# Optimization experiments

Measured on AMD Instinct MI355X. Metric: run time of the kernel, lower is better.

The kernel has to match this reference:

```python
import jax, jax.numpy as jnp
import numpy as np

N, E, NG = 10000, 160000, 64
HID, HEADS = 256, 4
NEG_SLOPE = 0.2


def setup_inputs() -> dict:
    key = jax.random.key(0)
    ks = jax.random.split(key, 20)
    s = 0.1
    inp = {
        "atom_features": jax.random.normal(ks[0], (N, 23), jnp.float32),
        "edge_index": jax.random.randint(ks[1], (2, E), 0, N),
        "batch": jnp.sort(jax.random.randint(ks[2], (N,), 0, NG)),
        "W1": jax.random.normal(ks[3], (23, HEADS * HID), jnp.float32) * s,
        "as1": jax.random.normal(ks[4], (HEADS, HID), jnp.float32) * s,
        "ad1": jax.random.normal(ks[5], (HEADS, HID), jnp.float32) * s,
        "b1": jnp.zeros((HEADS * HID,), jnp.float32),
        "W2": jax.random.normal(ks[6], (HEADS * HID, HEADS * HID), jnp.float32) * s,
        "as2": jax.random.normal(ks[7], (HEADS, HID), jnp.float32) * s,
        "ad2": jax.random.normal(ks[8], (HEADS, HID), jnp.float32) * s,
        "b2": jnp.zeros((HEADS * HID,), jnp.float32),
        "W3": jax.random.normal(ks[9], (HEADS * HID, HID), jnp.float32) * s,
        "as3": jax.random.normal(ks[10], (1, HID), jnp.float32) * s,
        "ad3": jax.random.normal(ks[11], (1, HID), jnp.float32) * s,
        "b3": jnp.zeros((HID,), jnp.float32),
        # MLP head
        "fc1_w": jax.random.normal(ks[12], (HID, HID // 2), jnp.float32) * s,
        "fc1_b": jnp.zeros((HID // 2,), jnp.float32),
        "fc2_w": jax.random.normal(ks[13], (HID // 2, 1), jnp.float32) * s,
        "fc2_b": jnp.zeros((1,), jnp.float32),
    }
    return inp


def gat_layer(x, W, att_src, att_dst, bias, src, dst, heads, ch):
    n = x.shape[0]
    h = (x @ W).reshape(n, heads, ch)                      # [N,H,C]
    a_s = jnp.sum(h * att_src, axis=-1)                    # [N,H]
    a_d = jnp.sum(h * att_dst, axis=-1)                    # [N,H]
    logits = jax.nn.leaky_relu(a_s[src] + a_d[dst], NEG_SLOPE)  # [E',H]
    m = jax.ops.segment_max(logits, dst, num_segments=n)
    m = jnp.where(jnp.isfinite(m), m, 0.0)
    e = jnp.exp(logits - m[dst])
    denom = jax.ops.segment_sum(e, dst, num_segments=n)
    alpha = e / (denom[dst] + 1e-16)                       # segment softmax over incoming edges
    out = jax.ops.segment_sum(alpha[:, :, None] * h[src], dst, num_segments=n)
    return out.reshape(n, heads * ch) + bias


def reference(atom_features, edge_index, batch,
              W1, as1, ad1, b1, W2, as2, ad2, b2, W3, as3, ad3, b3,
              fc1_w, fc1_b, fc2_w, fc2_b):
    n = atom_features.shape[0]
    loops = jnp.arange(n)
    src = jnp.concatenate([edge_index[0], loops])   # PyG GATConv adds self-loops
    dst = jnp.concatenate([edge_index[1], loops])

    x = jax.nn.elu(gat_layer(atom_features, W1, as1, ad1, b1, src, dst, HEADS, HID))
    x = jax.nn.elu(gat_layer(x, W2, as2, ad2, b2, src, dst, HEADS, HID))
    x = jax.nn.elu(gat_layer(x, W3, as3, ad3, b3, src, dst, 1, HID))
    # dropout: eval mode (training=False) -> identity

    # global mean pool over molecules
    sums = jax.ops.segment_sum(x, batch, num_segments=NG)
    counts = jax.ops.segment_sum(jnp.ones((n,), x.dtype), batch, num_segments=NG)
    features = sums / jnp.maximum(counts, 1.0)[:, None]    # [NG, HID]

    hmid = jax.nn.relu(features @ fc1_w + fc1_b)
    validity = hmid @ fc2_w + fc2_b                        # [NG, 1]
    return validity, features
```

## Files before the change

### kernel.cpp

```cpp
#include <hip/hip_runtime.h>
#include <hip/hip_bf16.h>
#include <math.h>

typedef unsigned short ushortT;
typedef __attribute__((ext_vector_type(8))) short short8;
typedef __attribute__((ext_vector_type(4))) float f32x4;

constexpr int NN   = 10000;
constexpr int EE   = 160000;
constexpr int ETOT = EE + NN;
constexpr int NG   = 64;
constexpr int HID  = 256;
constexpr int HEADS = 4;

__device__ __forceinline__ ushortT f2bf(float x) {
    __hip_bfloat16 h = __float2bfloat16(x);
    return *reinterpret_cast<ushortT*>(&h);
}
__device__ __forceinline__ float bf2f(ushortT x) {
    unsigned u = ((unsigned)x) << 16;
    return __uint_as_float(u);
}

__global__ void edge_count_kernel(const int* __restrict__ ei, int* __restrict__ cnt) {
    int e = blockIdx.x * blockDim.x + threadIdx.x;
    if (e >= ETOT) return;
    int dst = (e < EE) ? ei[EE + e] : (e - EE);
    atomicAdd(&cnt[dst], 1);
}

__global__ void scan_kernel(const int* __restrict__ cnt, int* __restrict__ row_ptr,
                            int* __restrict__ cursor) {
    __shared__ int part[256];
    int tid = threadIdx.x;
    const int chunk = (NN + 255) / 256;
    int s0 = tid * chunk;
    int s1 = min(NN, s0 + chunk);
    int sum = 0;
    for (int i = s0; i < s1; ++i) sum += cnt[i];
    part[tid] = sum;
    __syncthreads();
    for (int off = 1; off < 256; off <<= 1) {
        int v = (tid >= off) ? part[tid - off] : 0;
        __syncthreads();
        part[tid] += v;
        __syncthreads();
    }
    int run = (tid == 0) ? 0 : part[tid - 1];
    for (int i = s0; i < s1; ++i) {
        row_ptr[i] = run;
        cursor[i]  = run;
        run += cnt[i];
    }
    if (tid == 255) row_ptr[NN] = part[255];
}

__global__ void edge_fill_kernel(const int* __restrict__ ei, int* __restrict__ cursor,
                                 int* __restrict__ col_src) {
    int e = blockIdx.x * blockDim.x + threadIdx.x;
    if (e >= ETOT) return;
    int src, dst;
    if (e < EE) { src = ei[e]; dst = ei[EE + e]; }
    else        { src = dst = e - EE; }
    int pos = atomicAdd(&cursor[dst], 1);
    col_src[pos] = src;
}

__global__ void convert_wt(const float* __restrict__ W, ushortT* __restrict__ Wt,
                           int K, int N, int Kp) {
    __shared__ float t[32][33];
    int n0 = blockIdx.x * 32, k0 = blockIdx.y * 32;
    int tx = threadIdx.x, ty = threadIdx.y;
    for (int i = ty; i < 32; i += 8) {
        int k = k0 + i, n = n0 + tx;
        t[i][tx] = (k < K && n < N) ? W[(size_t)k * N + n] : 0.f;
    }
    __syncthreads();
    for (int i = ty; i < 32; i += 8) {
        int n = n0 + i, kp = k0 + tx;
        if (n < N && kp < Kp) Wt[(size_t)n * Kp + kp] = f2bf(t[tx][i]);
    }
}

__global__ void convert_atom(const float* __restrict__ a, ushortT* __restrict__ out) {
    int idx = blockIdx.x * 256 + threadIdx.x;
    if (idx >= NN * 32) return;
    int n = idx >> 5, k = idx & 31;
    out[idx] = (k < 23) ? f2bf(a[n * 23 + k]) : (ushortT)0;
}

__device__ __forceinline__ void gload_lds16(const ushortT* gsrc, ushortT* ldst) {
    __builtin_amdgcn_global_load_lds(
        (const __attribute__((address_space(1))) unsigned int*)gsrc,
        (__attribute__((address_space(3))) unsigned int*)ldst, 16, 0, 0);
}

__global__ __launch_bounds__(256, 2) void gemm_bf16(const ushortT* __restrict__ A,
                                                    const ushortT* __restrict__ Bt,
                                                    ushortT* __restrict__ C,
                                                    int M, int N, int K) {
    __shared__ ushortT lds[2][2][128][32];
    const int tid  = threadIdx.x;
    const int lane = tid & 63, w = tid >> 6;
    const int wm = w >> 1, wn = w & 1;
    const int row0 = blockIdx.y * 128;
    const int col0 = blockIdx.x * 128;
    const int nt = K >> 5;

    auto stage = [&](int buf, int t) {
        int k0 = t << 5;
        #pragma unroll
        for (int i = 0; i < 2; ++i) {
            int gbase = (w * 2 + i) * 64;
            int g = gbase + lane;
            int row = g >> 2;
            int sw = (row & 3) ^ ((row >> 2) & 3);
            int koff = (g & 3) ^ sw;
            int arow = min(row0 + row, M - 1);
            gload_lds16(A + (size_t)arow * K + k0 + koff * 8,
                        &lds[buf][0][0][0] + gbase * 8);
            int brow = col0 + row;
            gload_lds16(Bt + (size_t)brow * K + k0 + koff * 8,
                        &lds[buf][1][0][0] + gbase * 8);
        }
    };

    f32x4 acc[4][4] = {};
    const int lr = lane & 15, lk = lane >> 4;

    stage(0, 0);
    for (int t = 0; t < nt; ++t) {
        int buf = t & 1;
        __syncthreads();
        if (t + 1 < nt) stage(buf ^ 1, t + 1);
        short8 a[4], b[4];
        const ushortT* baseA = &lds[buf][0][0][0];
        const ushortT* baseB = &lds[buf][1][0][0];
        #pragma unroll
        for (int m = 0; m < 4; ++m) {
            int row = wm * 64 + m * 16 + lr;
            int sw = (row & 3) ^ ((row >> 2) & 3);
            a[m] = *(const short8*)(baseA + row * 32 + ((lk ^ sw) * 8));
        }
        #pragma unroll
        for (int n = 0; n < 4; ++n) {
            int row = wn * 64 + n * 16 + lr;
            int sw = (row & 3) ^ ((row >> 2) & 3);
            b[n] = *(const short8*)(baseB + row * 32 + ((lk ^ sw) * 8));
        }
        #pragma unroll
        for (int m = 0; m < 4; ++m)
            #pragma unroll
            for (int n = 0; n < 4; ++n)
                acc[m][n] = __builtin_amdgcn_mfma_f32_16x16x32_bf16(a[m], b[n], acc[m][n], 0, 0, 0);
    }

    #pragma unroll
    for (int m = 0; m < 4; ++m) {
        #pragma unroll
        for (int n = 0; n < 4; ++n) {
            int col = col0 + wn * 64 + n * 16 + lr;
            #pragma unroll
            for (int j = 0; j < 4; ++j) {
                int rowg = row0 + wm * 64 + m * 16 + lk * 4 + j;
                if (rowg < M) C[(size_t)rowg * N + col] = f2bf(acc[m][n][j]);
            }
        }
    }
}

__global__ void attn_dots2(const ushortT* __restrict__ h,
                           const float* __restrict__ att_s,
                           const float* __restrict__ att_d,
                           float* __restrict__ a_s, float* __restrict__ a_d,
                           int heads) {
    int wid  = (blockIdx.x * blockDim.x + threadIdx.x) >> 6;
    int lane = threadIdx.x & 63;
    int total = NN * heads;
    if (wid >= total) return;
    int n = wid / heads, hh = wid - n * heads;
    ushort4 v  = *(const ushort4*)(h + (size_t)n * heads * HID + hh * HID + lane * 4);
    float4 s4 = *(const float4*)(att_s + hh * HID + lane * 4);
    float4 d4 = *(const float4*)(att_d + hh * HID + lane * 4);
    float vx = bf2f(v.x), vy = bf2f(v.y), vz = bf2f(v.z), vw = bf2f(v.w);
    float as = vx * s4.x + vy * s4.y + vz * s4.z + vw * s4.w;
    float ad = vx * d4.x + vy * d4.y + vz * d4.z + vw * d4.w;
    #pragma unroll
    for (int off = 32; off > 0; off >>= 1) {
        as += __shfl_down(as, off);
        ad += __shfl_down(ad, off);
    }
    if (lane == 0) { a_s[wid] = as; a_d[wid] = ad; }
}

__global__ __launch_bounds__(256) void gat_aggregate(const ushortT* __restrict__ hfeat,
                                                     const float* __restrict__ a_s,
                                                     const float* __restrict__ a_d,
                                                     const int* __restrict__ row_ptr,
                                                     const int* __restrict__ col_src,
                                                     const float* __restrict__ bias,
                                                     float* __restrict__ outf,
                                                     ushortT* __restrict__ out16,
                                                     int heads) {
    const int i = blockIdx.x, tid = threadIdx.x;
    const int C = heads * HID;
    const int nch = heads;
    const int c0 = tid * nch;
    const int hh = c0 >> 8;
    const int start = row_ptr[i], end = row_ptr[i + 1];

    float ad_i[4];
    #pragma unroll
    for (int h2 = 0; h2 < 4; ++h2) ad_i[h2] = (h2 < heads) ? a_d[i * heads + h2] : 0.f;

    __shared__ float wbuf[4 * 128];
    __shared__ int   sbuf[128];
    __shared__ float red[4 * 256];
    float dpart[4] = {0.f, 0.f, 0.f, 0.f};
    float acc[4]   = {0.f, 0.f, 0.f, 0.f};
    for (int cb = start; cb < end; cb += 128) {
        int clen = min(128, end - cb);
        if (tid < clen) {
            int s = col_src[cb + tid];
            sbuf[tid] = s;
            #pragma unroll
            for (int h2 = 0; h2 < 4; ++h2) {
                if (h2 < heads) {
                    float l = a_s[s * heads + h2] + ad_i[h2];
                    l = (l >= 0.f) ? l : 0.2f * l;
                    float wv = expf(l);
                    wbuf[h2 * 128 + tid] = wv;
                    dpart[h2] += wv;
                }
            }
        }
        __syncthreads();
        if (nch == 4) {
            for (int e = 0; e < clen; ++e) {
                int s = sbuf[e];
                float wv = wbuf[hh * 128 + e];
                ushort4 v = *reinterpret_cast<const ushort4*>(hfeat + (size_t)s * C + c0);
                acc[0] += wv * bf2f(v.x); acc[1] += wv * bf2f(v.y);
                acc[2] += wv * bf2f(v.z); acc[3] += wv * bf2f(v.w);
            }
        } else {
            for (int e = 0; e < clen; ++e) {
                int s = sbuf[e];
                acc[0] += wbuf[e] * bf2f(hfeat[(size_t)s * C + c0]);
            }
        }
        __syncthreads();
    }
    for (int h2 = 0; h2 < heads; ++h2) red[h2 * 256 + tid] = dpart[h2];
    __syncthreads();
    for (int s2 = 128; s2 > 0; s2 >>= 1) {
        if (tid < s2)
            for (int h2 = 0; h2 < heads; ++h2)
                red[h2 * 256 + tid] += red[h2 * 256 + tid + s2];
        __syncthreads();
    }
    float denom = red[hh * 256] + 1e-16f;
    if (nch == 4) {
        ushort4 pk;
        float v0 = acc[0] / denom + bias[c0 + 0]; v0 = (v0 > 0.f) ? v0 : expm1f(v0);
        float v1 = acc[1] / denom + bias[c0 + 1]; v1 = (v1 > 0.f) ? v1 : expm1f(v1);
        float v2 = acc[2] / denom + bias[c0 + 2]; v2 = (v2 > 0.f) ? v2 : expm1f(v2);
        float v3 = acc[3] / denom + bias[c0 + 3]; v3 = (v3 > 0.f) ? v3 : expm1f(v3);
        pk.x = f2bf(v0); pk.y = f2bf(v1); pk.z = f2bf(v2); pk.w = f2bf(v3);
        *reinterpret_cast<ushort4*>(out16 + (size_t)i * C + c0) = pk;
    } else {
        float v = acc[0] / denom + bias[c0];
        v = (v > 0.f) ? v : expm1f(v);
        outf[(size_t)i * C + c0] = v;
    }
}

__global__ void pool_mlp(const float* __restrict__ x,
                         const int* __restrict__ batch,
                         const float* __restrict__ fc1_w,
                         const float* __restrict__ fc1_b,
                         const float* __restrict__ fc2_w,
                         const float* __restrict__ fc2_b,
                         float* __restrict__ out) {
    int g = blockIdx.x, tid = threadIdx.x;
    int lo = 0, hi = NN;
    while (lo < hi) { int mid = (lo + hi) >> 1; if (batch[mid] < g) lo = mid + 1; else hi = mid; }
    int s0 = lo;
    lo = 0; hi = NN;
    while (lo < hi) { int mid = (lo + hi) >> 1; if (batch[mid] < g + 1) lo = mid + 1; else hi = mid; }
    int s1 = lo;

    float acc = 0.f;
    for (int n = s0; n < s1; ++n) acc += x[(size_t)n * HID + tid];
    float cnt = (float)(s1 - s0);
    float feat = acc / fmaxf(cnt, 1.f);
    out[NG + g * HID + tid] = feat;

    __shared__ float fsh[HID];
    fsh[tid] = feat;
    __syncthreads();
    __shared__ float r2[128];
    if (tid < 128) {
        float a = fc1_b[tid];
        for (int c = 0; c < HID; ++c) a += fsh[c] * fc1_w[c * 128 + tid];
        a = fmaxf(a, 0.f);
        r2[tid] = a * fc2_w[tid];
    }
    __syncthreads();
    for (int s2 = 64; s2 > 0; s2 >>= 1) {
        if (tid < s2) r2[tid] += r2[tid + s2];
        __syncthreads();
    }
    if (tid == 0) out[g] = r2[0] + fc2_b[0];
}

extern "C" void kernel_launch(void* const* d_in, const int* in_sizes, int n_in,
                              void* d_out, int out_size, void* d_ws, size_t ws_size,
                              hipStream_t stream) {
    const float* atom  = (const float*)d_in[0];
    const int*   ei    = (const int*)  d_in[1];
    const int*   batch = (const int*)  d_in[2];
    const float* W1  = (const float*)d_in[3];
    const float* as1 = (const float*)d_in[4];
    const float* ad1 = (const float*)d_in[5];
    const float* b1  = (const float*)d_in[6];
    const float* W2  = (const float*)d_in[7];
    const float* as2 = (const float*)d_in[8];
    const float* ad2 = (const float*)d_in[9];
    const float* b2  = (const float*)d_in[10];
    const float* W3  = (const float*)d_in[11];
    const float* as3 = (const float*)d_in[12];
    const float* ad3 = (const float*)d_in[13];
    const float* b3  = (const float*)d_in[14];
    const float* fc1w = (const float*)d_in[15];
    const float* fc1b = (const float*)d_in[16];
    const float* fc2w = (const float*)d_in[17];
    const float* fc2b = (const float*)d_in[18];
    float* out = (float*)d_out;

    ushortT* h16  = (ushortT*)d_ws;
    ushortT* x16  = h16 + (size_t)NN * 1024;
    float*   x3   = (float*)(x16 + (size_t)NN * 1024);
    float*   a_s  = x3 + (size_t)NN * 256;
    float*   a_d  = a_s + (size_t)NN * HEADS;
    ushortT* wt1  = (ushortT*)(a_d + (size_t)NN * HEADS);
    ushortT* wt2  = wt1 + 1024 * 32;
    ushortT* wt3  = wt2 + 1024 * 1024;
    int*   cnt    = (int*)(wt3 + 256 * 1024);
    int*   rowp   = cnt + NN;
    int*   cursor = rowp + NN + 1;
    int*   col    = cursor + NN;

    hipMemsetAsync(cnt, 0, NN * sizeof(int), stream);
    edge_count_kernel<<<(ETOT + 255) / 256, 256, 0, stream>>>(ei, cnt);
    scan_kernel<<<1, 256, 0, stream>>>(cnt, rowp, cursor);
    edge_fill_kernel<<<(ETOT + 255) / 256, 256, 0, stream>>>(ei, cursor, col);

    dim3 cblk(32, 8);
    convert_atom<<<(NN * 32 + 255) / 256, 256, 0, stream>>>(atom, x16);
    convert_wt<<<dim3(32, 1),  cblk, 0, stream>>>(W1, wt1, 23,   1024, 32);
    convert_wt<<<dim3(32, 32), cblk, 0, stream>>>(W2, wt2, 1024, 1024, 1024);
    convert_wt<<<dim3(8, 32),  cblk, 0, stream>>>(W3, wt3, 1024, 256,  1024);

    dim3 blk(256);
    const int gy = (NN + 127) / 128;

    gemm_bf16<<<dim3(8, gy), blk, 0, stream>>>(x16, wt1, h16, NN, 1024, 32);
    attn_dots2<<<(NN * HEADS * 64 + 255) / 256, blk, 0, stream>>>(h16, as1, ad1, a_s, a_d, HEADS);
    gat_aggregate<<<NN, blk, 0, stream>>>(h16, a_s, a_d, rowp, col, b1, nullptr, x16, HEADS);

    gemm_bf16<<<dim3(8, gy), blk, 0, stream>>>(x16, wt2, h16, NN, 1024, 1024);
    attn_dots2<<<(NN * HEADS * 64 + 255) / 256, blk, 0, stream>>>(h16, as2, ad2, a_s, a_d, HEADS);
    gat_aggregate<<<NN, blk, 0, stream>>>(h16, a_s, a_d, rowp, col, b2, nullptr, x16, HEADS);

    gemm_bf16<<<dim3(2, gy), blk, 0, stream>>>(x16, wt3, h16, NN, 256, 1024);
    attn_dots2<<<(NN * 1 * 64 + 255) / 256, blk, 0, stream>>>(h16, as3, ad3, a_s, a_d, 1);
    gat_aggregate<<<NN, blk, 0, stream>>>(h16, a_s, a_d, rowp, col, b3, x3, nullptr, 1);

    pool_mlp<<<NG, blk, 0, stream>>>(x3, batch, fc1w, fc1b, fc2w, fc2b, out);
}
```

Baseline: 341.2 us.

## Fuse attention dots into GEMM epilogue and aggregate one node per wave

Removes the separate attn_dots2 kernel. The GEMM epilogue now computes each row's per-head source and destination attention dot products from the fp32 accumulators, reduces them with lane shuffles and atomically adds them into zeroed buffers. The aggregation kernel moves from one 256-thread block per node to one wavefront per node, four nodes per block. It uses wave-level barriers instead of __syncthreads, a shuffle reduction for the softmax denominator, and wider 16-element bf16 loads per lane. The cost is an extra memset per layer and atomics in the GEMM epilogue, and the dot products now come from unrounded accumulators, so numerics shift slightly.

```diff
diff --git a/kernel.cpp b/kernel.cpp
--- a/kernel.cpp
+++ b/kernel.cpp
@@ -98,6 +98,11 @@
 __global__ __launch_bounds__(256, 2) void gemm_bf16(const ushortT* __restrict__ A,
                                                     const ushortT* __restrict__ Bt,
                                                     ushortT* __restrict__ C,
+                                                    const float* __restrict__ att_s,
+                                                    const float* __restrict__ att_d,
+                                                    float* __restrict__ a_sp,
+                                                    float* __restrict__ a_dp,
+                                                    int adim,
                                                     int M, int N, int K) {
     __shared__ ushortT lds[2][2][128][32];
     const int tid  = threadIdx.x;
@@ -167,111 +172,152 @@
             }
         }
     }
-}
-
-__global__ void attn_dots2(const ushortT* __restrict__ h,
-                           const float* __restrict__ att_s,
-                           const float* __restrict__ att_d,
-                           float* __restrict__ a_s, float* __restrict__ a_d,
-                           int heads) {
-    int wid  = (blockIdx.x * blockDim.x + threadIdx.x) >> 6;
-    int lane = threadIdx.x & 63;
-    int total = NN * heads;
-    if (wid >= total) return;
-    int n = wid / heads, hh = wid - n * heads;
-    ushort4 v  = *(const ushort4*)(h + (size_t)n * heads * HID + hh * HID + lane * 4);
-    float4 s4 = *(const float4*)(att_s + hh * HID + lane * 4);
-    float4 d4 = *(const float4*)(att_d + hh * HID + lane * 4);
-    float vx = bf2f(v.x), vy = bf2f(v.y), vz = bf2f(v.z), vw = bf2f(v.w);
-    float as = vx * s4.x + vy * s4.y + vz * s4.z + vw * s4.w;
-    float ad = vx * d4.x + vy * d4.y + vz * d4.z + vw * d4.w;
-    #pragma unroll
-    for (int off = 32; off > 0; off >>= 1) {
-        as += __shfl_down(as, off);
-        ad += __shfl_down(ad, off);
-    }
-    if (lane == 0) { a_s[wid] = as; a_d[wid] = ad; }
-}
-
-__global__ __launch_bounds__(256) void gat_aggregate(const ushortT* __restrict__ hfeat,
-                                                     const float* __restrict__ a_s,
-                                                     const float* __restrict__ a_d,
-                                                     const int* __restrict__ row_ptr,
-                                                     const int* __restrict__ col_src,
-                                                     const float* __restrict__ bias,
-                                                     float* __restrict__ outf,
-                                                     ushortT* __restrict__ out16,
-                                                     int heads) {
-    const int i = blockIdx.x, tid = threadIdx.x;
+
+    {
+        const int colbase = col0 + wn * 64;
+        const int head = colbase >> 8;
+        float s_att[4], d_att[4];
+        #pragma unroll
+        for (int n = 0; n < 4; ++n) {
+            int col = colbase + n * 16 + lr;
+            s_att[n] = att_s[col];
+            d_att[n] = att_d[col];
+        }
+        #pragma unroll
+        for (int m = 0; m < 4; ++m) {
+            #pragma unroll
+            for (int j = 0; j < 4; ++j) {
+                float ps = acc[m][0][j] * s_att[0] + acc[m][1][j] * s_att[1]
+                         + acc[m][2][j] * s_att[2] + acc[m][3][j] * s_att[3];
+                float pd = acc[m][0][j] * d_att[0] + acc[m][1][j] * d_att[1]
+                         + acc[m][2][j] * d_att[2] + acc[m][3][j] * d_att[3];
+                #pragma unroll
+                for (int off = 1; off < 16; off <<= 1) {
+                    ps += __shfl_xor(ps, off);
+                    pd += __shfl_xor(pd, off);
+                }
+                if (lr == 0) {
+                    int rowg = row0 + wm * 64 + m * 16 + lk * 4 + j;
+                    if (rowg < M) {
+                        atomicAdd(a_sp + (size_t)rowg * adim + head, ps);
+                        atomicAdd(a_dp + (size_t)rowg * adim + head, pd);
+                    }
+                }
+            }
+        }
+    }
+}
+
+__global__ __launch_bounds__(256) void gat_aggregate_w(const ushortT* __restrict__ hfeat,
+                                                       const float* __restrict__ a_s,
+                                                       const float* __restrict__ a_d,
+                                                       const int* __restrict__ row_ptr,
+                                                       const int* __restrict__ col_src,
+                                                       const float* __restrict__ bias,
+                                                       float* __restrict__ outf,
+                                                       ushortT* __restrict__ out16,
+                                                       int heads) {
+    const int wv = threadIdx.x >> 6, lane = threadIdx.x & 63;
+    const int i = blockIdx.x * 4 + wv;
+    if (i >= NN) return;
     const int C = heads * HID;
-    const int nch = heads;
-    const int c0 = tid * nch;
+    const int nch = C >> 6;
+    const int c0 = lane * nch;
     const int hh = c0 >> 8;
     const int start = row_ptr[i], end = row_ptr[i + 1];
 
-    float ad_i[4];
+    __shared__ float wsh[4][64][4];
+    __shared__ int   ssh[4][64];
+
+    float acc[16];
     #pragma unroll
-    for (int h2 = 0; h2 < 4; ++h2) ad_i[h2] = (h2 < heads) ? a_d[i * heads + h2] : 0.f;
-
-    __shared__ float wbuf[4 * 128];
-    __shared__ int   sbuf[128];
-    __shared__ float red[4 * 256];
-    float dpart[4] = {0.f, 0.f, 0.f, 0.f};
-    float acc[4]   = {0.f, 0.f, 0.f, 0.f};
-    for (int cb = start; cb < end; cb += 128) {
-        int clen = min(128, end - cb);
-        if (tid < clen) {
-            int s = col_src[cb + tid];
-            sbuf[tid] = s;
-            #pragma unroll
-            for (int h2 = 0; h2 < 4; ++h2) {
-                if (h2 < heads) {
-                    float l = a_s[s * heads + h2] + ad_i[h2];
-                    l = (l >= 0.f) ? l : 0.2f * l;
-                    float wv = expf(l);
-                    wbuf[h2 * 128 + tid] = wv;
-                    dpart[h2] += wv;
+    for (int c = 0; c < 16; ++c) acc[c] = 0.f;
+    float den4[4] = {0.f, 0.f, 0.f, 0.f};
+
+    for (int cb = start; cb < end; cb += 64) {
+        int clen = min(64, end - cb);
+        if (lane < clen) {
+            int s = col_src[cb + lane];
+            ssh[wv][lane] = s;
+            if (heads == 4) {
+                float4 as4 = *(const float4*)(a_s + (size_t)s * 4);
+                float4 ad4 = *(const float4*)(a_d + (size_t)i * 4);
+                float l0 = as4.x + ad4.x; l0 = (l0 >= 0.f) ? l0 : 0.2f * l0;
+                float l1 = as4.y + ad4.y; l1 = (l1 >= 0.f) ? l1 : 0.2f * l1;
+                float l2 = as4.z + ad4.z; l2 = (l2 >= 0.f) ? l2 : 0.2f * l2;
+                float l3 = as4.w + ad4.w; l3 = (l3 >= 0.f) ? l3 : 0.2f * l3;
+                float w0 = expf(l0), w1 = expf(l1), w2 = expf(l2), w3 = expf(l3);
+                *reinterpret_cast<float4*>(&wsh[wv][lane][0]) = make_float4(w0, w1, w2, w3);
+                den4[0] += w0; den4[1] += w1; den4[2] += w2; den4[3] += w3;
+            } else {
+                float l0 = a_s[s] + a_d[i]; l0 = (l0 >= 0.f) ? l0 : 0.2f * l0;
+                float w0 = expf(l0);
+                wsh[wv][lane][0] = w0;
+                den4[0] += w0;
+            }
+        }
+        __builtin_amdgcn_wave_barrier();
+        if (nch == 16) {
+            for (int e = 0; e < clen; ++e) {
+                int s = ssh[wv][e];
+                float wgt = wsh[wv][e][hh];
+                const ushortT* p = hfeat + (size_t)s * C + c0;
+                short8 v0 = *(const short8*)p;
+                short8 v1 = *(const short8*)(p + 8);
+                #pragma unroll
+                for (int j = 0; j < 8; ++j) {
+                    acc[j]     += wgt * bf2f((ushortT)v0[j]);
+                    acc[8 + j] += wgt * bf2f((ushortT)v1[j]);
                 }
-            }
-        }
-        __syncthreads();
-        if (nch == 4) {
-            for (int e = 0; e < clen; ++e) {
-                int s = sbuf[e];
-                float wv = wbuf[hh * 128 + e];
-                ushort4 v = *reinterpret_cast<const ushort4*>(hfeat + (size_t)s * C + c0);
-                acc[0] += wv * bf2f(v.x); acc[1] += wv * bf2f(v.y);
-                acc[2] += wv * bf2f(v.z); acc[3] += wv * bf2f(v.w);
             }
         } else {
             for (int e = 0; e < clen; ++e) {
-                int s = sbuf[e];
-                acc[0] += wbuf[e] * bf2f(hfeat[(size_t)s * C + c0]);
+                int s = ssh[wv][e];
+                float wgt = wsh[wv][e][0];
+                const ushortT* p = hfeat + (size_t)s * C + c0;
+                ushort4 v = *(const ushort4*)p;
+                acc[0] += wgt * bf2f(v.x); acc[1] += wgt * bf2f(v.y);
+                acc[2] += wgt * bf2f(v.z); acc[3] += wgt * bf2f(v.w);
             }
         }
-        __syncthreads();
-    }
-    for (int h2 = 0; h2 < heads; ++h2) red[h2 * 256 + tid] = dpart[h2];
-    __syncthreads();
-    for (int s2 = 128; s2 > 0; s2 >>= 1) {
-        if (tid < s2)
-            for (int h2 = 0; h2 < heads; ++h2)
-                red[h2 * 256 + tid] += red[h2 * 256 + tid + s2];
-        __syncthreads();
-    }
-    float denom = red[hh * 256] + 1e-16f;
-    if (nch == 4) {
-        ushort4 pk;
-        float v0 = acc[0] / denom + bias[c0 + 0]; v0 = (v0 > 0.f) ? v0 : expm1f(v0);
-        float v1 = acc[1] / denom + bias[c0 + 1]; v1 = (v1 > 0.f) ? v1 : expm1f(v1);
-        float v2 = acc[2] / denom + bias[c0 + 2]; v2 = (v2 > 0.f) ? v2 : expm1f(v2);
-        float v3 = acc[3] / denom + bias[c0 + 3]; v3 = (v3 > 0.f) ? v3 : expm1f(v3);
-        pk.x = f2bf(v0); pk.y = f2bf(v1); pk.z = f2bf(v2); pk.w = f2bf(v3);
-        *reinterpret_cast<ushort4*>(out16 + (size_t)i * C + c0) = pk;
+        __builtin_amdgcn_wave_barrier();
+    }
+
+    if (heads == 4) {
+        #pragma unroll
+        for (int off = 1; off < 64; off <<= 1) {
+            den4[0] += __shfl_xor(den4[0], off);
+            den4[1] += __shfl_xor(den4[1], off);
+            den4[2] += __shfl_xor(den4[2], off);
+            den4[3] += __shfl_xor(den4[3], off);
+        }
     } else {
-        float v = acc[0] / denom + bias[c0];
-        v = (v > 0.f) ? v : expm1f(v);
-        outf[(size_t)i * C + c0] = v;
+        #pragma unroll
+        for (int off = 1; off < 64; off <<= 1) den4[0] += __shfl_xor(den4[0], off);
+    }
+    float den = den4[0];
+    if (heads == 4) {
+        den = (hh == 0) ? den4[0] : (hh == 1) ? den4[1] : (hh == 2) ? den4[2] : den4[3];
+    }
+    float inv = 1.f / (den + 1e-16f);
+
+    if (heads == 4) {
+        ushortT pk[16];
+        #pragma unroll
+        for (int c = 0; c < 16; ++c) {
+            float v = acc[c] * inv + bias[c0 + c];
+            v = (v > 0.f) ? v : expm1f(v);
+            pk[c] = f2bf(v);
+        }
+        *reinterpret_cast<short8*>(out16 + (size_t)i * C + c0)     = *reinterpret_cast<short8*>(&pk[0]);
+        *reinterpret_cast<short8*>(out16 + (size_t)i * C + c0 + 8) = *reinterpret_cast<short8*>(&pk[8]);
+    } else {
+        float4 o;
+        float v0 = acc[0] * inv + bias[c0 + 0]; o.x = (v0 > 0.f) ? v0 : expm1f(v0);
+        float v1 = acc[1] * inv + bias[c0 + 1]; o.y = (v1 > 0.f) ? v1 : expm1f(v1);
+        float v2 = acc[2] * inv + bias[c0 + 2]; o.z = (v2 > 0.f) ? v2 : expm1f(v2);
+        float v3 = acc[3] * inv + bias[c0 + 3]; o.w = (v3 > 0.f) ? v3 : expm1f(v3);
+        *reinterpret_cast<float4*>(outf + (size_t)i * C + c0) = o;
     }
 }
 
@@ -364,18 +410,19 @@
 
     dim3 blk(256);
     const int gy = (NN + 127) / 128;
-
-    gemm_bf16<<<dim3(8, gy), blk, 0, stream>>>(x16, wt1, h16, NN, 1024, 32);
-    attn_dots2<<<(NN * HEADS * 64 + 255) / 256, blk, 0, stream>>>(h16, as1, ad1, a_s, a_d, HEADS);
-    gat_aggregate<<<NN, blk, 0, stream>>>(h16, a_s, a_d, rowp, col, b1, nullptr, x16, HEADS);
-
-    gemm_bf16<<<dim3(8, gy), blk, 0, stream>>>(x16, wt2, h16, NN, 1024, 1024);
-    attn_dots2<<<(NN * HEADS * 64 + 255) / 256, blk, 0, stream>>>(h16, as2, ad2, a_s, a_d, HEADS);
-    gat_aggregate<<<NN, blk, 0, stream>>>(h16, a_s, a_d, rowp, col, b2, nullptr, x16, HEADS);
-
-    gemm_bf16<<<dim3(2, gy), blk, 0, stream>>>(x16, wt3, h16, NN, 256, 1024);
-    attn_dots2<<<(NN * 1 * 64 + 255) / 256, blk, 0, stream>>>(h16, as3, ad3, a_s, a_d, 1);
-    gat_aggregate<<<NN, blk, 0, stream>>>(h16, a_s, a_d, rowp, col, b3, x3, nullptr, 1);
+    const int gagg = (NN + 3) / 4;
+
+    hipMemsetAsync(a_s, 0, (size_t)NN * 2 * HEADS * sizeof(float), stream);
+    gemm_bf16<<<dim3(8, gy), blk, 0, stream>>>(x16, wt1, h16, as1, ad1, a_s, a_d, HEADS, NN, 1024, 32);
+    gat_aggregate_w<<<gagg, blk, 0, stream>>>(h16, a_s, a_d, rowp, col, b1, nullptr, x16, HEADS);
+
+    hipMemsetAsync(a_s, 0, (size_t)NN * 2 * HEADS * sizeof(float), stream);
+    gemm_bf16<<<dim3(8, gy), blk, 0, stream>>>(x16, wt2, h16, as2, ad2, a_s, a_d, HEADS, NN, 1024, 1024);
+    gat_aggregate_w<<<gagg, blk, 0, stream>>>(h16, a_s, a_d, rowp, col, b2, nullptr, x16, HEADS);
+
+    hipMemsetAsync(a_s, 0, (size_t)NN * 2 * HEADS * sizeof(float), stream);
+    gemm_bf16<<<dim3(2, gy), blk, 0, stream>>>(x16, wt3, h16, as3, ad3, a_s, a_d, 1, NN, 256, 1024);
+    gat_aggregate_w<<<gagg, blk, 0, stream>>>(h16, a_s, a_d, rowp, col, b3, x3, nullptr, 1);
 
     pool_mlp<<<NG, blk, 0, stream>>>(x3, batch, fc1w, fc1b, fc2w, fc2b, out);
 }
```

After: 358.3 us. +5.0%, slower.

## Fold attention projections into weights and fuse next-layer dots into aggregation

Applied to the files above, without the earlier changes.

Precomputes W·att_src and W·att_dst so the per-node attention scores for the next layer are computed inside the aggregation epilogue, accumulated with atomics, instead of by a separate dot kernel over the GEMM output. This removes the attn_dots kernels and a full re-read of the projected features per layer. It also rewrites aggregation as two wavefronts per node, each loading 8 neighbors' 8-channel vectors with no LDS or block-level syncs. The scores now come from fp32 activations rather than the bf16-rounded GEMM output, which slightly changes numerics, and the scheme adds atomics and memsets.

```diff
diff --git a/kernel.cpp b/kernel.cpp
--- a/kernel.cpp
+++ b/kernel.cpp
@@ -89,6 +89,43 @@
     out[idx] = (k < 23) ? f2bf(a[n * 23 + k]) : (ushortT)0;
 }
 
+__global__ void proj_att(const float* __restrict__ W,
+                         const float* __restrict__ atts,
+                         const float* __restrict__ attd,
+                         float* __restrict__ wsv,
+                         int K, int heads) {
+    const int nout = 2 * heads;
+    int gw   = (blockIdx.x * blockDim.x + threadIdx.x) >> 6;
+    int lane = threadIdx.x & 63;
+    if (gw >= K * nout) return;
+    int k = gw / nout, o = gw - k * nout;
+    int h = (o >= heads) ? (o - heads) : o;
+    const float* att  = ((o >= heads) ? attd : atts) + h * HID;
+    const float* wrow = W + (size_t)k * (heads * HID) + h * HID;
+    float4 w4 = *(const float4*)(wrow + lane * 4);
+    float4 a4 = *(const float4*)(att + lane * 4);
+    float s = w4.x * a4.x + w4.y * a4.y + w4.z * a4.z + w4.w * a4.w;
+    #pragma unroll
+    for (int off = 1; off < 64; off <<= 1) s += __shfl_xor(s, off);
+    if (lane == 0) wsv[(size_t)k * nout + o] = s;
+}
+
+__global__ void dots1_kernel(const float* __restrict__ atom,
+                             const float* __restrict__ wsv1,
+                             float* __restrict__ a_s, float* __restrict__ a_d) {
+    int n = blockIdx.x * 256 + threadIdx.x;
+    if (n >= NN) return;
+    float a[8] = {0.f, 0.f, 0.f, 0.f, 0.f, 0.f, 0.f, 0.f};
+    #pragma unroll
+    for (int k = 0; k < 23; ++k) {
+        float x = atom[n * 23 + k];
+        #pragma unroll
+        for (int o = 0; o < 8; ++o) a[o] += x * wsv1[k * 8 + o];
+    }
+    #pragma unroll
+    for (int h = 0; h < 4; ++h) { a_s[n * 4 + h] = a[h]; a_d[n * 4 + h] = a[4 + h]; }
+}
+
 __device__ __forceinline__ void gload_lds16(const ushortT* gsrc, ushortT* ldst) {
     __builtin_amdgcn_global_load_lds(
         (const __attribute__((address_space(1))) unsigned int*)gsrc,
@@ -169,110 +206,145 @@
     }
 }
 
-__global__ void attn_dots2(const ushortT* __restrict__ h,
-                           const float* __restrict__ att_s,
-                           const float* __restrict__ att_d,
-                           float* __restrict__ a_s, float* __restrict__ a_d,
-                           int heads) {
-    int wid  = (blockIdx.x * blockDim.x + threadIdx.x) >> 6;
+template<int NOUT>
+__global__ __launch_bounds__(256) void gat_agg4(const ushortT* __restrict__ hfeat,
+                                                const float* __restrict__ a_s,
+                                                const float* __restrict__ a_d,
+                                                const int* __restrict__ rowp,
+                                                const int* __restrict__ colv,
+                                                const float* __restrict__ bias,
+                                                ushortT* __restrict__ out16,
+                                                const float* __restrict__ wsv,
+                                                float* __restrict__ as_next,
+                                                float* __restrict__ ad_next) {
+    int gw   = (blockIdx.x * blockDim.x + threadIdx.x) >> 6;
     int lane = threadIdx.x & 63;
-    int total = NN * heads;
-    if (wid >= total) return;
-    int n = wid / heads, hh = wid - n * heads;
-    ushort4 v  = *(const ushort4*)(h + (size_t)n * heads * HID + hh * HID + lane * 4);
-    float4 s4 = *(const float4*)(att_s + hh * HID + lane * 4);
-    float4 d4 = *(const float4*)(att_d + hh * HID + lane * 4);
-    float vx = bf2f(v.x), vy = bf2f(v.y), vz = bf2f(v.z), vw = bf2f(v.w);
-    float as = vx * s4.x + vy * s4.y + vz * s4.z + vw * s4.w;
-    float ad = vx * d4.x + vy * d4.y + vz * d4.z + vw * d4.w;
+    int i = gw >> 1, p = gw & 1;
+    if (i >= NN) return;
+    const int c0 = p * 512 + lane * 8;
+    const int hh = c0 >> 8;
+    const int start = rowp[i], end = rowp[i + 1];
+    const float adh = a_d[i * 4 + hh];
+
+    float acc[8] = {0.f, 0.f, 0.f, 0.f, 0.f, 0.f, 0.f, 0.f};
+    float den = 0.f;
+    for (int e0 = start; e0 < end; e0 += 8) {
+        const int mcnt = end - e0;
+        int sidx[8];
+        #pragma unroll
+        for (int j = 0; j < 8; ++j) sidx[j] = colv[(j < mcnt) ? (e0 + j) : e0];
+        short8 v[8];
+        #pragma unroll
+        for (int j = 0; j < 8; ++j)
+            v[j] = *(const short8*)(hfeat + (size_t)sidx[j] * 1024 + c0);
+        float asv[8];
+        #pragma unroll
+        for (int j = 0; j < 8; ++j) asv[j] = a_s[sidx[j] * 4 + hh];
+        float wv[8];
+        #pragma unroll
+        for (int j = 0; j < 8; ++j) {
+            float l = asv[j] + adh;
+            l = (l >= 0.f) ? l : 0.2f * l;
+            wv[j] = (j < mcnt) ? expf(l) : 0.f;
+            den += wv[j];
+        }
+        #pragma unroll
+        for (int j = 0; j < 8; ++j) {
+            #pragma unroll
+            for (int c = 0; c < 8; ++c)
+                acc[c] += wv[j] * bf2f((ushortT)v[j][c]);
+        }
+    }
+    float inv = 1.f / (den + 1e-16f);
+    float vout[8];
+    ushortT pk[8];
     #pragma unroll
-    for (int off = 32; off > 0; off >>= 1) {
-        as += __shfl_down(as, off);
-        ad += __shfl_down(ad, off);
-    }
-    if (lane == 0) { a_s[wid] = as; a_d[wid] = ad; }
-}
-
-__global__ __launch_bounds__(256) void gat_aggregate(const ushortT* __restrict__ hfeat,
-                                                     const float* __restrict__ a_s,
-                                                     const float* __restrict__ a_d,
-                                                     const int* __restrict__ row_ptr,
-                                                     const int* __restrict__ col_src,
-                                                     const float* __restrict__ bias,
-                                                     float* __restrict__ outf,
-                                                     ushortT* __restrict__ out16,
-                                                     int heads) {
-    const int i = blockIdx.x, tid = threadIdx.x;
-    const int C = heads * HID;
-    const int nch = heads;
-    const int c0 = tid * nch;
-    const int hh = c0 >> 8;
-    const int start = row_ptr[i], end = row_ptr[i + 1];
-
-    float ad_i[4];
-    #pragma unroll
-    for (int h2 = 0; h2 < 4; ++h2) ad_i[h2] = (h2 < heads) ? a_d[i * heads + h2] : 0.f;
-
-    __shared__ float wbuf[4 * 128];
-    __shared__ int   sbuf[128];
-    __shared__ float red[4 * 256];
-    float dpart[4] = {0.f, 0.f, 0.f, 0.f};
-    float acc[4]   = {0.f, 0.f, 0.f, 0.f};
-    for (int cb = start; cb < end; cb += 128) {
-        int clen = min(128, end - cb);
-        if (tid < clen) {
-            int s = col_src[cb + tid];
-            sbuf[tid] = s;
-            #pragma unroll
-            for (int h2 = 0; h2 < 4; ++h2) {
-                if (h2 < heads) {
-                    float l = a_s[s * heads + h2] + ad_i[h2];
-                    l = (l >= 0.f) ? l : 0.2f * l;
-                    float wv = expf(l);
-                    wbuf[h2 * 128 + tid] = wv;
-                    dpart[h2] += wv;
-                }
+    for (int c = 0; c < 8; ++c) {
+        float v = acc[c] * inv + bias[c0 + c];
+        v = (v > 0.f) ? v : expm1f(v);
+        vout[c] = v;
+        pk[c] = f2bf(v);
+    }
+    *reinterpret_cast<short8*>(out16 + (size_t)i * 1024 + c0) =
+        *reinterpret_cast<const short8*>(pk);
+
+    if (NOUT > 0) {
+        float ps[NOUT];
+        #pragma unroll
+        for (int o = 0; o < NOUT; ++o) {
+            float t = 0.f;
+            #pragma unroll
+            for (int c = 0; c < 8; ++c) t += vout[c] * wsv[(size_t)(c0 + c) * NOUT + o];
+            ps[o] = t;
+        }
+        #pragma unroll
+        for (int off = 1; off < 64; off <<= 1) {
+            #pragma unroll
+            for (int o = 0; o < NOUT; ++o) ps[o] += __shfl_xor(ps[o], off);
+        }
+        if (lane == 0) {
+            constexpr int NH = NOUT / 2;
+            #pragma unroll
+            for (int o = 0; o < NH; ++o) {
+                atomicAdd(as_next + (size_t)i * NH + o, ps[o]);
+                atomicAdd(ad_next + (size_t)i * NH + o, ps[NH + o]);
             }
         }
-        __syncthreads();
-        if (nch == 4) {
-            for (int e = 0; e < clen; ++e) {
-                int s = sbuf[e];
-                float wv = wbuf[hh * 128 + e];
-                ushort4 v = *reinterpret_cast<const ushort4*>(hfeat + (size_t)s * C + c0);
-                acc[0] += wv * bf2f(v.x); acc[1] += wv * bf2f(v.y);
-                acc[2] += wv * bf2f(v.z); acc[3] += wv * bf2f(v.w);
-            }
-        } else {
-            for (int e = 0; e < clen; ++e) {
-                int s = sbuf[e];
-                acc[0] += wbuf[e] * bf2f(hfeat[(size_t)s * C + c0]);
-            }
-        }
-        __syncthreads();
-    }
-    for (int h2 = 0; h2 < heads; ++h2) red[h2 * 256 + tid] = dpart[h2];
-    __syncthreads();
-    for (int s2 = 128; s2 > 0; s2 >>= 1) {
-        if (tid < s2)
-            for (int h2 = 0; h2 < heads; ++h2)
-                red[h2 * 256 + tid] += red[h2 * 256 + tid + s2];
-        __syncthreads();
-    }
-    float denom = red[hh * 256] + 1e-16f;
-    if (nch == 4) {
-        ushort4 pk;
-        float v0 = acc[0] / denom + bias[c0 + 0]; v0 = (v0 > 0.f) ? v0 : expm1f(v0);
-        float v1 = acc[1] / denom + bias[c0 + 1]; v1 = (v1 > 0.f) ? v1 : expm1f(v1);
-        float v2 = acc[2] / denom + bias[c0 + 2]; v2 = (v2 > 0.f) ? v2 : expm1f(v2);
-        float v3 = acc[3] / denom + bias[c0 + 3]; v3 = (v3 > 0.f) ? v3 : expm1f(v3);
-        pk.x = f2bf(v0); pk.y = f2bf(v1); pk.z = f2bf(v2); pk.w = f2bf(v3);
-        *reinterpret_cast<ushort4*>(out16 + (size_t)i * C + c0) = pk;
-    } else {
-        float v = acc[0] / denom + bias[c0];
-        v = (v > 0.f) ? v : expm1f(v);
-        outf[(size_t)i * C + c0] = v;
-    }
+    }
+}
+
+__global__ __launch_bounds__(256) void gat_agg1(const ushortT* __restrict__ hfeat,
+                                                const float* __restrict__ a_s,
+                                                const float* __restrict__ a_d,
+                                                const int* __restrict__ rowp,
+                                                const int* __restrict__ colv,
+                                                const float* __restrict__ bias,
+                                                float* __restrict__ outf) {
+    int gw   = (blockIdx.x * blockDim.x + threadIdx.x) >> 6;
+    int lane = threadIdx.x & 63;
+    int i = gw;
+    if (i >= NN) return;
+    const int c0 = lane * 4;
+    const int start = rowp[i], end = rowp[i + 1];
+    const float adh = a_d[i];
+
+    float acc[4] = {0.f, 0.f, 0.f, 0.f};
+    float den = 0.f;
+    for (int e0 = start; e0 < end; e0 += 8) {
+        const int mcnt = end - e0;
+        int sidx[8];
+        #pragma unroll
+        for (int j = 0; j < 8; ++j) sidx[j] = colv[(j < mcnt) ? (e0 + j) : e0];
+        ushort4 v[8];
+        #pragma unroll
+        for (int j = 0; j < 8; ++j)
+            v[j] = *(const ushort4*)(hfeat + (size_t)sidx[j] * 256 + c0);
+        float asv[8];
+        #pragma unroll
+        for (int j = 0; j < 8; ++j) asv[j] = a_s[sidx[j]];
+        float wv[8];
+        #pragma unroll
+        for (int j = 0; j < 8; ++j) {
+            float l = asv[j] + adh;
+            l = (l >= 0.f) ? l : 0.2f * l;
+            wv[j] = (j < mcnt) ? expf(l) : 0.f;
+            den += wv[j];
+        }
+        #pragma unroll
+        for (int j = 0; j < 8; ++j) {
+            acc[0] += wv[j] * bf2f(v[j].x);
+            acc[1] += wv[j] * bf2f(v[j].y);
+            acc[2] += wv[j] * bf2f(v[j].z);
+            acc[3] += wv[j] * bf2f(v[j].w);
+        }
+    }
+    float inv = 1.f / (den + 1e-16f);
+    float4 o4;
+    float v0 = acc[0] * inv + bias[c0 + 0]; o4.x = (v0 > 0.f) ? v0 : expm1f(v0);
+    float v1 = acc[1] * inv + bias[c0 + 1]; o4.y = (v1 > 0.f) ? v1 : expm1f(v1);
+    float v2 = acc[2] * inv + bias[c0 + 2]; o4.z = (v2 > 0.f) ? v2 : expm1f(v2);
+    float v3 = acc[3] * inv + bias[c0 + 3]; o4.w = (v3 > 0.f) ? v3 : expm1f(v3);
+    *reinterpret_cast<float4*>(outf + (size_t)i * 256 + c0) = o4;
 }
 
 __global__ void pool_mlp(const float* __restrict__ x,
@@ -341,9 +413,14 @@
     ushortT* h16  = (ushortT*)d_ws;
     ushortT* x16  = h16 + (size_t)NN * 1024;
     float*   x3   = (float*)(x16 + (size_t)NN * 1024);
-    float*   a_s  = x3 + (size_t)NN * 256;
-    float*   a_d  = a_s + (size_t)NN * HEADS;
-    ushortT* wt1  = (ushortT*)(a_d + (size_t)NN * HEADS);
+    float*   asA  = x3 + (size_t)NN * 256;
+    float*   adA  = asA + (size_t)NN * 4;
+    float*   asB  = adA + (size_t)NN * 4;
+    float*   adB  = asB + (size_t)NN * 4;
+    float*   wsv1 = adB + (size_t)NN * 4;
+    float*   wsv2 = wsv1 + 23 * 8;
+    float*   wsv3 = wsv2 + 1024 * 8;
+    ushortT* wt1  = (ushortT*)(wsv3 + 1024 * 2);
     ushortT* wt2  = wt1 + 1024 * 32;
     ushortT* wt3  = wt2 + 1024 * 1024;
     int*   cnt    = (int*)(wt3 + 256 * 1024);
@@ -362,20 +439,27 @@
     convert_wt<<<dim3(32, 32), cblk, 0, stream>>>(W2, wt2, 1024, 1024, 1024);
     convert_wt<<<dim3(8, 32),  cblk, 0, stream>>>(W3, wt3, 1024, 256,  1024);
 
+    proj_att<<<(23 * 8 * 64 + 255) / 256, 256, 0, stream>>>(W1, as1, ad1, wsv1, 23, 4);
+    proj_att<<<(1024 * 8 * 64 + 255) / 256, 256, 0, stream>>>(W2, as2, ad2, wsv2, 1024, 4);
+    proj_att<<<(1024 * 2 * 64 + 255) / 256, 256, 0, stream>>>(W3, as3, ad3, wsv3, 1024, 1);
+
+    dots1_kernel<<<(NN + 255) / 256, 256, 0, stream>>>(atom, wsv1, asA, adA);
+    hipMemsetAsync(asB, 0, (size_t)NN * 8 * sizeof(float), stream);
+
     dim3 blk(256);
     const int gy = (NN + 127) / 128;
 
     gemm_bf16<<<dim3(8, gy), blk, 0, stream>>>(x16, wt1, h16, NN, 1024, 32);
-    attn_dots2<<<(NN * HEADS * 64 + 255) / 256, blk, 0, stream>>>(h16, as1, ad1, a_s, a_d, HEADS);
-    gat_aggregate<<<NN, blk, 0, stream>>>(h16, a_s, a_d, rowp, col, b1, nullptr, x16, HEADS);
+    gat_agg4<8><<<(NN * 2 * 64 + 255) / 256, blk, 0, stream>>>(h16, asA, adA, rowp, col,
+                                                               b1, x16, wsv2, asB, adB);
+    hipMemsetAsync(asA, 0, (size_t)NN * 8 * sizeof(float), stream);
 
     gemm_bf16<<<dim3(8, gy), blk, 0, stream>>>(x16, wt2, h16, NN, 1024, 1024);
-    attn_dots2<<<(NN * HEADS * 64 + 255) / 256, blk, 0, stream>>>(h16, as2, ad2, a_s, a_d, HEADS);
-    gat_aggregate<<<NN, blk, 0, stream>>>(h16, a_s, a_d, rowp, col, b2, nullptr, x16, HEADS);
+    gat_agg4<2><<<(NN * 2 * 64 + 255) / 256, blk, 0, stream>>>(h16, asB, adB, rowp, col,
+                                                               b2, x16, wsv3, asA, adA);
 
     gemm_bf16<<<dim3(2, gy), blk, 0, stream>>>(x16, wt3, h16, NN, 256, 1024);
-    attn_dots2<<<(NN * 1 * 64 + 255) / 256, blk, 0, stream>>>(h16, as3, ad3, a_s, a_d, 1);
-    gat_aggregate<<<NN, blk, 0, stream>>>(h16, a_s, a_d, rowp, col, b3, x3, nullptr, 1);
+    gat_agg1<<<(NN * 64 + 255) / 256, blk, 0, stream>>>(h16, asA, adA, rowp, col, b3, x3);
 
     pool_mlp<<<NG, blk, 0, stream>>>(x3, batch, fc1w, fc1b, fc2w, fc2b, out);
 }
```

Result: slower. 367.9 us (+7.8%).
